# Kernel optimization log

Hardware: AMD Instinct MI355X
Metric: run time of the kernel (lower is better)

Reference implementation:

```python
import jax, jax.numpy as jnp
import numpy as np

T, N, E, F_IN, C = 8, 50000, 800000, 64, 64


def setup_inputs() -> dict:
    key = jax.random.key(0)
    ks = jax.random.split(key, 32)
    inp = {
        "x": jax.random.normal(ks[0], (T, N, F_IN), dtype=jnp.float32),
        "edge_index": jax.random.randint(ks[1], (2, E), 0, N, dtype=jnp.int32),
        "edge_weight": jax.random.uniform(ks[2], (E,), dtype=jnp.float32),
    }
    s = 0.05
    names = ["xz", "hz", "xr", "hr", "xh", "hh"]
    for i, nm in enumerate(names):
        cin = F_IN if nm[0] == "x" else C
        inp[f"W{nm}0"] = jax.random.normal(ks[3 + 3 * i], (cin, C), dtype=jnp.float32) * s
        inp[f"W{nm}1"] = jax.random.normal(ks[4 + 3 * i], (cin, C), dtype=jnp.float32) * s
        inp[f"b{nm}"] = jax.random.normal(ks[5 + 3 * i], (C,), dtype=jnp.float32) * s
    inp["W_lin"] = jax.random.normal(ks[30], (C, 1), dtype=jnp.float32) * s
    inp["b_lin"] = jax.random.normal(ks[31], (1,), dtype=jnp.float32) * s
    return inp


def reference(x, edge_index, edge_weight,
              Wxz0, Wxz1, bxz, Whz0, Whz1, bhz,
              Wxr0, Wxr1, bxr, Whr0, Whr1, bhr,
              Wxh0, Wxh1, bxh, Whh0, Whh1, bhh,
              W_lin, b_lin):
    src, dst = edge_index[0], edge_index[1]
    n = x.shape[1]
    # sym-normalized L_hat = -D^{-1/2} A D^{-1/2} (ChebConv, lambda_max=2)
    deg = jnp.zeros((n,), x.dtype).at[src].add(edge_weight)
    dinv = jnp.where(deg > 0, jax.lax.rsqrt(jnp.maximum(deg, 1e-12)), 0.0)
    nw = -edge_weight * dinv[src] * dinv[dst]  # (E,)

    def cheb(v, W0, W1, b):
        # K=2 Chebyshev: v @ W0 + (L_hat v) @ W1 + b ; v: (T, N, Cin)
        msgs = nw[None, :, None] * v[:, src, :]          # (T, E, Cin)
        tx1 = jnp.zeros_like(v).at[:, dst, :].add(msgs)  # scatter-add over nodes
        return v @ W0 + tx1 @ W1 + b

    H = jnp.zeros(x.shape[:2] + (Whz0.shape[0],), x.dtype)  # H=None -> zeros
    Z = jax.nn.sigmoid(cheb(x, Wxz0, Wxz1, bxz) + cheb(H, Whz0, Whz1, bhz))
    R = jax.nn.sigmoid(cheb(x, Wxr0, Wxr1, bxr) + cheb(H, Whr0, Whr1, bhr))
    Ht = jnp.tanh(cheb(x, Wxh0, Wxh1, bxh) + cheb(R * H, Whh0, Whh1, bhh))
    H = Z * H + (1.0 - Z) * Ht
    h = jax.nn.relu(H)
    return h @ W_lin + b_lin
```

## Files before the change

kernel.cpp:

```cpp
#include <hip/hip_runtime.h>

#define T_ 8
#define N_ 50000
#define E_ 800000
#define C_ 64
#define OVF_CAP 131072
#define NB 196
#define NBLK 256
#define EPB 3125
#define SCN (2 * NB * NBLK)
#define SCAN_TILES 49

typedef __attribute__((ext_vector_type(8))) short bf16x8;
typedef __attribute__((ext_vector_type(4))) float f32x4;

__device__ inline short f2bf(float f) {
    union { float f; unsigned int u; } v; v.f = f;
    unsigned int u = v.u + 0x7FFFu + ((v.u >> 16) & 1u);
    return (short)(u >> 16);
}
__device__ inline float bf2f_lo(unsigned int u) {
    union { unsigned int u; float f; } v; v.u = u << 16;
    return v.f;
}
__device__ inline float bf2f_hi(unsigned int u) {
    union { unsigned int u; float f; } v; v.u = u & 0xffff0000u;
    return v.f;
}

__device__ inline void xcvt_step(int id, const float* __restrict__ x,
                                 unsigned short* __restrict__ xb) {
    int c8 = id & 7;
    int t = (id >> 3) & 7;
    int n = id >> 6;
    const float* xr = x + ((long long)t * N_ + n) * C_ + c8 * 8;
    float4 a = *(const float4*)(xr);
    float4 b = *(const float4*)(xr + 4);
    bf16x8 o;
    o[0] = f2bf(a.x); o[1] = f2bf(a.y); o[2] = f2bf(a.z); o[3] = f2bf(a.w);
    o[4] = f2bf(b.x); o[5] = f2bf(b.y); o[6] = f2bf(b.z); o[7] = f2bf(b.w);
    *(bf16x8*)(xb + (long long)id * 8) = o;
}

__global__ __launch_bounds__(256) void prep_kernel(
        const int* __restrict__ src, const int* __restrict__ dst,
        int* __restrict__ counts,
        const float* __restrict__ x, unsigned short* __restrict__ xb,
        const float* __restrict__ Wz0, const float* __restrict__ Wz1,
        const float* __restrict__ Wh0, const float* __restrict__ Wh1,
        short* __restrict__ swz) {
    if (blockIdx.x < NBLK) {
        __shared__ int h[2 * NB];
        int t = threadIdx.x;
        for (int i = t; i < 2 * NB; i += 256) h[i] = 0;
        __syncthreads();
        int e0 = blockIdx.x * EPB;
        for (int j = t; j < EPB; j += 256) {
            int e = e0 + j;
            atomicAdd(&h[src[e] >> 8], 1);
            atomicAdd(&h[NB + (dst[e] >> 8)], 1);
        }
        __syncthreads();
        for (int i = t; i < 2 * NB; i += 256)
            counts[i * NBLK + blockIdx.x] = h[i];
    } else if (blockIdx.x < NBLK + 12500) {
        int id = (blockIdx.x - NBLK) * 256 + threadIdx.x;
        xcvt_step(id, x, xb);
    } else {
        int idx = (blockIdx.x - NBLK - 12500) * 256 + threadIdx.x;
        int j = idx & 7;
        int lane = (idx >> 3) & 63;
        int kb = (idx >> 9) & 1;
        int c = (idx >> 10) & 3;
        int mat = idx >> 12;
        const float* W = (mat == 0) ? Wz0 : (mat == 1) ? Wz1 : (mat == 2) ? Wh0 : Wh1;
        int k = kb * 32 + (lane >> 4) * 8 + j;
        int n = c * 16 + (lane & 15);
        swz[idx] = f2bf(W[k * 64 + n]);
    }
}

__global__ __launch_bounds__(1024) void scan_a_kernel(int* __restrict__ cnts,
                                                      int* __restrict__ tsum) {
    __shared__ int wsum[16];
    int tid = threadIdx.x, lane = tid & 63, wid = tid >> 6;
    int i0 = blockIdx.x * 2048 + tid * 2;
    int v0 = cnts[i0], v1 = cnts[i0 + 1];
    int orig = v0 + v1;
    int v = orig;
#pragma unroll
    for (int off = 1; off < 64; off <<= 1) {
        int u = __shfl_up(v, off);
        if (lane >= off) v += u;
    }
    if (lane == 63) wsum[wid] = v;
    __syncthreads();
    if (wid == 0) {
        int s = (lane < 16) ? wsum[lane] : 0;
#pragma unroll
        for (int off = 1; off < 16; off <<= 1) {
            int u = __shfl_up(s, off);
            if (lane >= off) s += u;
        }
        if (lane < 16) wsum[lane] = s;
    }
    __syncthreads();
    int wpre = wid ? wsum[wid - 1] : 0;
    int ex = wpre + v - orig;
    cnts[i0] = ex;
    cnts[i0 + 1] = ex + v0;
    if (tid == 0) tsum[blockIdx.x] = wsum[15];
}

__global__ __launch_bounds__(1024) void scan_b_kernel(const int* __restrict__ tsum,
                                                      int* __restrict__ cnts,
                                                      int* __restrict__ ovfcnt) {
    __shared__ int soff[SCAN_TILES];
    int tid = threadIdx.x, lane = tid & 63, wid = tid >> 6;
    if (blockIdx.x == 0 && tid == 0) *ovfcnt = 0;
    if (wid == 0) {
        int own = (lane < SCAN_TILES) ? tsum[lane] : 0;
        int s = own;
#pragma unroll
        for (int off = 1; off < 64; off <<= 1) {
            int u = __shfl_up(s, off);
            if (lane >= off) s += u;
        }
        if (lane < SCAN_TILES) soff[lane] = s - own;
    }
    __syncthreads();
    int off = soff[blockIdx.x];
    int i0 = blockIdx.x * 2048 + tid;
    cnts[i0] += off;
    cnts[i0 + 1024] += off;
}

__global__ __launch_bounds__(1024) void scatter_kernel(
        const int* __restrict__ src, const int* __restrict__ dst,
        const float* __restrict__ w, const int* __restrict__ scn,
        int2* __restrict__ rec) {
    __shared__ int h[512];
    __shared__ int delta[512];
    __shared__ int wsum[8];
    __shared__ int2 lrec[2 * EPB];
    int t = threadIdx.x, lane = t & 63, wid = t >> 6;
    int c = blockIdx.x;
    if (t < 512) h[t] = 0;
    __syncthreads();
    int e0 = c * EPB;
    for (int j = t; j < EPB; j += 1024) {
        int e = e0 + j;
        atomicAdd(&h[src[e] >> 8], 1);
        atomicAdd(&h[NB + (dst[e] >> 8)], 1);
    }
    __syncthreads();
    int v = (t < 512) ? h[t] : 0;
    int s2 = v;
#pragma unroll
    for (int off = 1; off < 64; off <<= 1) {
        int u = __shfl_up(s2, off);
        if (lane >= off) s2 += u;
    }
    if (lane == 63 && wid < 8) wsum[wid] = s2;
    __syncthreads();
    if (t == 0) {
        int r = 0;
#pragma unroll
        for (int i = 0; i < 8; ++i) { int x2 = wsum[i]; wsum[i] = r; r += x2; }
    }
    __syncthreads();
    int ex = (t < 512) ? (wsum[wid] + s2 - v) : 0;
    int gb = (t < 2 * NB) ? scn[t * NBLK + c] : 0;
    __syncthreads();
    if (t < 512) { delta[t] = gb - ex; h[t] = ex; }
    __syncthreads();
    int lb196 = h[NB];
    __syncthreads();
    for (int j = t; j < EPB; j += 1024) {
        int e = e0 + j;
        int s = src[e], d = dst[e];
        int wv = __float_as_int(w[e]);
        int p0 = atomicAdd(&h[s >> 8], 1);
        lrec[p0] = make_int2(s, wv);
        int p1 = atomicAdd(&h[NB + (d >> 8)], 1);
        lrec[p1] = make_int2(s | ((d & 255) << 16) | ((d >> 8) << 24), wv);
    }
    __syncthreads();
    for (int j = t; j < 2 * EPB; j += 1024) {
        int2 r = lrec[j];
        int i = (j >= lb196) ? (NB + ((unsigned)r.x >> 24)) : ((r.x & 0xffff) >> 8);
        rec[delta[i] + j] = r;
    }
}

__global__ __launch_bounds__(1024) void degw_kernel(
        const int2* __restrict__ rec, const int* __restrict__ scn,
        float* __restrict__ degw) {
    __shared__ float acc[256];
    int t = threadIdx.x, b = blockIdx.x;
    if (t < 256) acc[t] = 0.f;
    __syncthreads();
    int s0 = scn[b * NBLK];
    int s1 = scn[(b + 1) * NBLK];
    for (int j = s0 + t; j < s1; j += 1024) {
        int2 r = rec[j];
        atomicAdd(&acc[r.x & 255], __int_as_float(r.y));
    }
    __syncthreads();
    int node = b * 256 + t;
    if (t < 256 && node < N_) degw[node] = acc[t];
}

__global__ __launch_bounds__(1024) void esbuild_kernel(
        const int2* __restrict__ rec, const int* __restrict__ scn,
        const float* __restrict__ degw, int* __restrict__ cnt,
        int2* __restrict__ es, int cap,
        int* __restrict__ ovfcnt, int4* __restrict__ ovf) {
    __shared__ int cl[256];
    __shared__ float di[256];
    int t = threadIdx.x, b = blockIdx.x;
    int node = b * 256 + t;
    if (t < 256) {
        cl[t] = 0;
        float dd = (node < N_) ? degw[node] : 0.f;
        di[t] = dd > 0.f ? rsqrtf(fmaxf(dd, 1e-12f)) : 0.f;
    }
    __syncthreads();
    int s0 = scn[(NB + b) * NBLK];
    int s1 = (b == NB - 1) ? 2 * E_ : scn[(NB + b + 1) * NBLK];
    for (int j = s0 + t; j < s1; j += 1024) {
        int2 r = rec[j];
        int s = r.x & 0xffff;
        int dl = (r.x >> 16) & 255;
        float ds = degw[s];
        float is = ds > 0.f ? rsqrtf(fmaxf(ds, 1e-12f)) : 0.f;
        float nwv = -__int_as_float(r.y) * is * di[dl];
        int rank = atomicAdd(&cl[dl], 1);
        int d = b * 256 + dl;
        if (rank < cap) {
            es[d * cap + rank] = make_int2(s, __float_as_int(nwv));
        } else {
            int op = atomicAdd(ovfcnt, 1);
            if (op < OVF_CAP) ovf[op] = make_int4(d, s, __float_as_int(nwv), 0);
        }
    }
    __syncthreads();
    if (t < 256 && node < N_) cnt[node] = cl[t];
}

#define ACC8(W, V)                                                       \
    acc[0] += (W) * bf2f_lo((V).x); acc[1] += (W) * bf2f_hi((V).x);      \
    acc[2] += (W) * bf2f_lo((V).y); acc[3] += (W) * bf2f_hi((V).y);      \
    acc[4] += (W) * bf2f_lo((V).z); acc[5] += (W) * bf2f_hi((V).z);      \
    acc[6] += (W) * bf2f_lo((V).w); acc[7] += (W) * bf2f_hi((V).w);

__global__ __launch_bounds__(256) void gather_node_kernel(
        const int* __restrict__ cnt, const int2* __restrict__ es, int cap,
        const int* __restrict__ ovfcnt, const int4* __restrict__ ovf,
        const unsigned short* __restrict__ xb, const short* __restrict__ swz,
        const float* __restrict__ bxz, const float* __restrict__ bhz,
        const float* __restrict__ bxh, const float* __restrict__ bhh,
        const float* __restrict__ Wlin, const float* __restrict__ blin,
        float* __restrict__ out, int boff) {
    __shared__ unsigned short ltx[32 * 72];
    __shared__ float laz[2][16][65];

    int lane = threadIdx.x & 63;
    int wid = threadIdx.x >> 6;
    int base = (blockIdx.x + boff) * 4;

    {
        int d = base + wid;
        int t = lane >> 3;
        int oct = lane & 7;
        int2 pk = (lane < cap) ? es[d * cap + lane] : make_int2(0, 0);
        int m = cnt[d];
        int mb = m < cap ? m : cap;

        float acc[8] = {0.f, 0.f, 0.f, 0.f, 0.f, 0.f, 0.f, 0.f};
        const unsigned short* xbase = xb + lane * 8;
        int k = 0;
        for (; k + 3 < mb; k += 4) {
            int s0 = __shfl(pk.x, k);
            int s1 = __shfl(pk.x, k + 1);
            int s2 = __shfl(pk.x, k + 2);
            int s3 = __shfl(pk.x, k + 3);
            uint4 v0 = *(const uint4*)(xbase + (long long)s0 * 512);
            uint4 v1 = *(const uint4*)(xbase + (long long)s1 * 512);
            uint4 v2 = *(const uint4*)(xbase + (long long)s2 * 512);
            uint4 v3 = *(const uint4*)(xbase + (long long)s3 * 512);
            float w0 = __int_as_float(__shfl(pk.y, k));
            float w1 = __int_as_float(__shfl(pk.y, k + 1));
            float w2 = __int_as_float(__shfl(pk.y, k + 2));
            float w3 = __int_as_float(__shfl(pk.y, k + 3));
            ACC8(w0, v0);
            ACC8(w1, v1);
            ACC8(w2, v2);
            ACC8(w3, v3);
        }
        for (; k < mb; ++k) {
            int s0 = __shfl(pk.x, k);
            float w0 = __int_as_float(__shfl(pk.y, k));
            uint4 v0 = *(const uint4*)(xbase + (long long)s0 * 512);
            ACC8(w0, v0);
        }
        if (m > cap) {
            int oc = *ovfcnt;
            if (oc > OVF_CAP) oc = OVF_CAP;
            for (int i = 0; i < oc; ++i) {
                int4 o = ovf[i];
                if (o.x == d) {
                    float w0 = __int_as_float(o.z);
                    uint4 v0 = *(const uint4*)(xbase + (long long)o.y * 512);
                    ACC8(w0, v0);
                }
            }
        }
        uint4 ob;
        ob.x = (unsigned int)(unsigned short)f2bf(acc[0]) |
               ((unsigned int)(unsigned short)f2bf(acc[1]) << 16);
        ob.y = (unsigned int)(unsigned short)f2bf(acc[2]) |
               ((unsigned int)(unsigned short)f2bf(acc[3]) << 16);
        ob.z = (unsigned int)(unsigned short)f2bf(acc[4]) |
               ((unsigned int)(unsigned short)f2bf(acc[5]) << 16);
        ob.w = (unsigned int)(unsigned short)f2bf(acc[6]) |
               ((unsigned int)(unsigned short)f2bf(acc[7]) << 16);
        int r = wid * 8 + t;
        *(uint4*)(ltx + r * 72 + oct * 8) = ob;
    }
    __syncthreads();

    int mt = wid >> 1;
    int g = wid & 1;
    int c16 = lane & 15;
    int kq = lane >> 4;
    int r_blk = mt * 16 + c16;
    const unsigned short* xr = xb + (long long)(base * 8 + r_blk) * C_ + kq * 8;
    bf16x8 ax0 = *(const bf16x8*)(xr);
    bf16x8 ax1 = *(const bf16x8*)(xr + 32);
    bf16x8 at0 = *(const bf16x8*)(ltx + r_blk * 72 + kq * 8);
    bf16x8 at1 = *(const bf16x8*)(ltx + r_blk * 72 + 32 + kq * 8);

    const float* bA = g ? bxh : bxz;
    const float* bB = g ? bhh : bhz;
    const short* wA = swz + (2 * g) * 4096 + lane * 8;
    const short* wB = swz + (2 * g + 1) * 4096 + lane * 8;

    f32x4 a4[4];
#pragma unroll
    for (int c = 0; c < 4; ++c) {
        int col = c * 16 + c16;
        float bv = bA[col] + bB[col];
        a4[c] = (f32x4){bv, bv, bv, bv};
    }
#pragma unroll
    for (int c = 0; c < 4; ++c) {
        bf16x8 bA0 = *(const bf16x8*)(wA + (c * 2 + 0) * 512);
        bf16x8 bA1 = *(const bf16x8*)(wA + (c * 2 + 1) * 512);
        bf16x8 bB0 = *(const bf16x8*)(wB + (c * 2 + 0) * 512);
        bf16x8 bB1 = *(const bf16x8*)(wB + (c * 2 + 1) * 512);
        a4[c] = __builtin_amdgcn_mfma_f32_16x16x32_bf16(ax0, bA0, a4[c], 0, 0, 0);
        a4[c] = __builtin_amdgcn_mfma_f32_16x16x32_bf16(ax1, bA1, a4[c], 0, 0, 0);
        a4[c] = __builtin_amdgcn_mfma_f32_16x16x32_bf16(at0, bB0, a4[c], 0, 0, 0);
        a4[c] = __builtin_amdgcn_mfma_f32_16x16x32_bf16(at1, bB1, a4[c], 0, 0, 0);
    }

    if (g == 0) {
#pragma unroll
        for (int c = 0; c < 4; ++c)
#pragma unroll
            for (int r = 0; r < 4; ++r)
                laz[mt][kq * 4 + r][c * 16 + c16] = a4[c][r];
    }
    __syncthreads();
    if (g == 1) {
        float part[4] = {0.f, 0.f, 0.f, 0.f};
#pragma unroll
        for (int c = 0; c < 4; ++c) {
            int col = c * 16 + c16;
            float wl = Wlin[col];
#pragma unroll
            for (int r = 0; r < 4; ++r) {
                float a = laz[mt][kq * 4 + r][col];
                float b = a4[c][r];
                float z = 1.f / (1.f + __expf(-a));
                float aa = fabsf(b);
                float e = __expf(-2.f * aa);
                float ht = copysignf((1.f - e) / (1.f + e), b);
                float h = fmaxf((1.f - z) * ht, 0.f);
                part[r] += h * wl;
            }
        }
#pragma unroll
        for (int m = 1; m <= 8; m <<= 1) {
#pragma unroll
            for (int r = 0; r < 4; ++r) part[r] += __shfl_xor(part[r], m);
        }
        if (c16 == 0) {
            float bl = blin[0];
#pragma unroll
            for (int r = 0; r < 4; ++r) {
                int rb = mt * 16 + kq * 4 + r;
                out[(long long)(rb & 7) * N_ + base + (rb >> 3)] = part[r] + bl;
            }
        }
    }
}

extern "C" void kernel_launch(void* const* d_in, const int* in_sizes, int n_in,
                              void* d_out, int out_size, void* d_ws, size_t ws_size,
                              hipStream_t stream) {
    const float* x    = (const float*)d_in[0];
    const int*   ei   = (const int*)d_in[1];
    const float* w    = (const float*)d_in[2];
    const float* Wxz0 = (const float*)d_in[3];
    const float* Wxz1 = (const float*)d_in[4];
    const float* bxz  = (const float*)d_in[5];
    const float* bhz  = (const float*)d_in[8];
    const float* Wxh0 = (const float*)d_in[15];
    const float* Wxh1 = (const float*)d_in[16];
    const float* bxh  = (const float*)d_in[17];
    const float* bhh  = (const float*)d_in[20];
    const float* Wlin = (const float*)d_in[21];
    const float* blin = (const float*)d_in[22];
    float* out = (float*)d_out;

    const int* src = ei;
    const int* dst = ei + E_;

    char* ws = (char*)d_ws;
    size_t off = 0;
    auto alloc = [&](size_t bytes) {
        char* p = ws + off;
        off = (off + bytes + 511) & ~(size_t)511;
        return p;
    };
    short* swz         = (short*)alloc(4 * 4096 * sizeof(short));
    float* degw        = (float*)alloc((size_t)N_ * 4);
    int*   cnt         = (int*)alloc((size_t)N_ * 4);
    int*   ovfcnt      = (int*)alloc(512);
    int4*  ovf         = (int4*)alloc((size_t)OVF_CAP * 16);
    int*   counts      = (int*)alloc((size_t)SCN * 4);
    int*   tsum        = (int*)alloc((size_t)SCAN_TILES * 4);
    int2*  rec         = (int2*)alloc((size_t)2 * E_ * 8);
    unsigned short* xb = (unsigned short*)alloc((size_t)T_ * N_ * C_ * 2);
    size_t fixed = off;

    int cap = 16;
    for (int c : {64, 48, 32, 24}) {
        if (fixed + (size_t)N_ * c * 8 + 512 <= ws_size) { cap = c; break; }
    }
    int2* es = (int2*)alloc((size_t)N_ * cap * 8);

    prep_kernel<<<NBLK + 12500 + 64, 256, 0, stream>>>(
        src, dst, counts, x, xb, Wxz0, Wxz1, Wxh0, Wxh1, swz);

    scan_a_kernel<<<SCAN_TILES, 1024, 0, stream>>>(counts, tsum);
    scan_b_kernel<<<SCAN_TILES, 1024, 0, stream>>>(tsum, counts, ovfcnt);

    scatter_kernel<<<NBLK, 1024, 0, stream>>>(src, dst, w, counts, rec);

    degw_kernel<<<NB, 1024, 0, stream>>>(rec, counts, degw);

    esbuild_kernel<<<NB, 1024, 0, stream>>>(rec, counts, degw, cnt,
                                            es, cap, ovfcnt, ovf);

    gather_node_kernel<<<6250, 256, 0, stream>>>(
        cnt, es, cap, ovfcnt, ovf, xb, swz,
        bxz, bhz, bxh, bhh, Wlin, blin, out, 0);
    gather_node_kernel<<<6250, 256, 0, stream>>>(
        cnt, es, cap, ovfcnt, ovf, xb, swz,
        bxz, bhz, bxh, bhh, Wlin, blin, out, 6250);
}
```

Baseline: 367.9 us.

## Replace global scan with atomic bucket cursors and fuse scatter into prep

```diff
diff --git a/kernel.cpp b/kernel.cpp
--- a/kernel.cpp
+++ b/kernel.cpp
@@ -4,12 +4,11 @@
 #define N_ 50000
 #define E_ 800000
 #define C_ 64
-#define OVF_CAP 131072
+#define OVF_CAP 65536
 #define NB 196
 #define NBLK 256
 #define EPB 3125
-#define SCN (2 * NB * NBLK)
-#define SCAN_TILES 49
+#define BCAP 6144
 
 typedef __attribute__((ext_vector_type(8))) short bf16x8;
 typedef __attribute__((ext_vector_type(4))) float f32x4;
@@ -42,32 +41,89 @@
     *(bf16x8*)(xb + (long long)id * 8) = o;
 }
 
-__global__ __launch_bounds__(256) void prep_kernel(
+__global__ __launch_bounds__(1024) void mega_prep_kernel(
         const int* __restrict__ src, const int* __restrict__ dst,
-        int* __restrict__ counts,
+        const float* __restrict__ w,
+        unsigned long long* __restrict__ cursor,
+        int* __restrict__ ovfAcnt, int4* __restrict__ ovfA,
+        int2* __restrict__ rec,
         const float* __restrict__ x, unsigned short* __restrict__ xb,
         const float* __restrict__ Wz0, const float* __restrict__ Wz1,
         const float* __restrict__ Wh0, const float* __restrict__ Wh1,
         short* __restrict__ swz) {
+    int t = threadIdx.x;
     if (blockIdx.x < NBLK) {
-        __shared__ int h[2 * NB];
-        int t = threadIdx.x;
-        for (int i = t; i < 2 * NB; i += 256) h[i] = 0;
-        __syncthreads();
-        int e0 = blockIdx.x * EPB;
-        for (int j = t; j < EPB; j += 256) {
+        __shared__ int h[512];
+        __shared__ int delta[512];
+        __shared__ int wsum[16];
+        __shared__ unsigned long long gres[NB];
+        __shared__ int2 lrec[2 * EPB];
+        int lane = t & 63, wid = t >> 6;
+        int c = blockIdx.x;
+        if (t < 512) h[t] = 0;
+        __syncthreads();
+        int e0 = c * EPB;
+        for (int j = t; j < EPB; j += 1024) {
             int e = e0 + j;
             atomicAdd(&h[src[e] >> 8], 1);
             atomicAdd(&h[NB + (dst[e] >> 8)], 1);
         }
         __syncthreads();
-        for (int i = t; i < 2 * NB; i += 256)
-            counts[i * NBLK + blockIdx.x] = h[i];
-    } else if (blockIdx.x < NBLK + 12500) {
-        int id = (blockIdx.x - NBLK) * 256 + threadIdx.x;
+        int v = (t < 512) ? h[t] : 0;
+        if (t < NB) {
+            unsigned long long add =
+                ((unsigned long long)(unsigned)h[NB + t] << 32) | (unsigned)h[t];
+            gres[t] = atomicAdd(&cursor[t], add);
+        }
+        int s2 = v;
+#pragma unroll
+        for (int off = 1; off < 64; off <<= 1) {
+            int u = __shfl_up(s2, off);
+            if (lane >= off) s2 += u;
+        }
+        if (lane == 63) wsum[wid] = s2;
+        __syncthreads();
+        if (t == 0) {
+            int r = 0;
+#pragma unroll
+            for (int i = 0; i < 16; ++i) { int x2 = wsum[i]; wsum[i] = r; r += x2; }
+        }
+        __syncthreads();
+        int ex = wsum[wid] + s2 - v;
+        if (t < 512) {
+            int gb = (t < NB) ? (int)(gres[t] & 0xffffffffULL)
+                              : (int)(gres[t - NB] >> 32);
+            delta[t] = gb - ex;
+            h[t] = ex;
+        }
+        __syncthreads();
+        for (int j = t; j < EPB; j += 1024) {
+            int e = e0 + j;
+            int s = src[e], d = dst[e];
+            int wv = __float_as_int(w[e]);
+            int p0 = atomicAdd(&h[s >> 8], 1);
+            lrec[p0] = make_int2(s, wv);
+            int p1 = atomicAdd(&h[NB + (d >> 8)], 1);
+            lrec[p1] = make_int2(s | ((d & 255) << 16) | ((d >> 8) << 24), wv);
+        }
+        __syncthreads();
+        for (int j = t; j < 2 * EPB; j += 1024) {
+            int2 r = lrec[j];
+            int isd = (j >= EPB);
+            int i = isd ? (NB + (int)((unsigned)r.x >> 24)) : ((r.x & 0xffff) >> 8);
+            int rel = delta[i] + j;
+            if (rel < BCAP) {
+                rec[(long long)i * BCAP + rel] = r;
+            } else {
+                int op = atomicAdd(ovfAcnt, 1);
+                if (op < OVF_CAP) ovfA[op] = make_int4(isd, r.x, r.y, 0);
+            }
+        }
+    } else if (blockIdx.x < NBLK + 3125) {
+        int id = (blockIdx.x - NBLK) * 1024 + t;
         xcvt_step(id, x, xb);
     } else {
-        int idx = (blockIdx.x - NBLK - 12500) * 256 + threadIdx.x;
+        int idx = (blockIdx.x - NBLK - 3125) * 1024 + t;
         int j = idx & 7;
         int lane = (idx >> 3) & 63;
         int kb = (idx >> 9) & 1;
@@ -80,131 +136,32 @@
     }
 }
 
-__global__ __launch_bounds__(1024) void scan_a_kernel(int* __restrict__ cnts,
-                                                      int* __restrict__ tsum) {
-    __shared__ int wsum[16];
-    int tid = threadIdx.x, lane = tid & 63, wid = tid >> 6;
-    int i0 = blockIdx.x * 2048 + tid * 2;
-    int v0 = cnts[i0], v1 = cnts[i0 + 1];
-    int orig = v0 + v1;
-    int v = orig;
-#pragma unroll
-    for (int off = 1; off < 64; off <<= 1) {
-        int u = __shfl_up(v, off);
-        if (lane >= off) v += u;
-    }
-    if (lane == 63) wsum[wid] = v;
-    __syncthreads();
-    if (wid == 0) {
-        int s = (lane < 16) ? wsum[lane] : 0;
-#pragma unroll
-        for (int off = 1; off < 16; off <<= 1) {
-            int u = __shfl_up(s, off);
-            if (lane >= off) s += u;
-        }
-        if (lane < 16) wsum[lane] = s;
-    }
-    __syncthreads();
-    int wpre = wid ? wsum[wid - 1] : 0;
-    int ex = wpre + v - orig;
-    cnts[i0] = ex;
-    cnts[i0 + 1] = ex + v0;
-    if (tid == 0) tsum[blockIdx.x] = wsum[15];
-}
-
-__global__ __launch_bounds__(1024) void scan_b_kernel(const int* __restrict__ tsum,
-                                                      int* __restrict__ cnts,
-                                                      int* __restrict__ ovfcnt) {
-    __shared__ int soff[SCAN_TILES];
-    int tid = threadIdx.x, lane = tid & 63, wid = tid >> 6;
-    if (blockIdx.x == 0 && tid == 0) *ovfcnt = 0;
-    if (wid == 0) {
-        int own = (lane < SCAN_TILES) ? tsum[lane] : 0;
-        int s = own;
-#pragma unroll
-        for (int off = 1; off < 64; off <<= 1) {
-            int u = __shfl_up(s, off);
-            if (lane >= off) s += u;
-        }
-        if (lane < SCAN_TILES) soff[lane] = s - own;
-    }
-    __syncthreads();
-    int off = soff[blockIdx.x];
-    int i0 = blockIdx.x * 2048 + tid;
-    cnts[i0] += off;
-    cnts[i0 + 1024] += off;
-}
-
-__global__ __launch_bounds__(1024) void scatter_kernel(
-        const int* __restrict__ src, const int* __restrict__ dst,
-        const float* __restrict__ w, const int* __restrict__ scn,
-        int2* __restrict__ rec) {
-    __shared__ int h[512];
-    __shared__ int delta[512];
-    __shared__ int wsum[8];
-    __shared__ int2 lrec[2 * EPB];
-    int t = threadIdx.x, lane = t & 63, wid = t >> 6;
-    int c = blockIdx.x;
-    if (t < 512) h[t] = 0;
-    __syncthreads();
-    int e0 = c * EPB;
-    for (int j = t; j < EPB; j += 1024) {
-        int e = e0 + j;
-        atomicAdd(&h[src[e] >> 8], 1);
-        atomicAdd(&h[NB + (dst[e] >> 8)], 1);
-    }
-    __syncthreads();
-    int v = (t < 512) ? h[t] : 0;
-    int s2 = v;
-#pragma unroll
-    for (int off = 1; off < 64; off <<= 1) {
-        int u = __shfl_up(s2, off);
-        if (lane >= off) s2 += u;
-    }
-    if (lane == 63 && wid < 8) wsum[wid] = s2;
-    __syncthreads();
-    if (t == 0) {
-        int r = 0;
-#pragma unroll
-        for (int i = 0; i < 8; ++i) { int x2 = wsum[i]; wsum[i] = r; r += x2; }
-    }
-    __syncthreads();
-    int ex = (t < 512) ? (wsum[wid] + s2 - v) : 0;
-    int gb = (t < 2 * NB) ? scn[t * NBLK + c] : 0;
-    __syncthreads();
-    if (t < 512) { delta[t] = gb - ex; h[t] = ex; }
-    __syncthreads();
-    int lb196 = h[NB];
-    __syncthreads();
-    for (int j = t; j < EPB; j += 1024) {
-        int e = e0 + j;
-        int s = src[e], d = dst[e];
-        int wv = __float_as_int(w[e]);
-        int p0 = atomicAdd(&h[s >> 8], 1);
-        lrec[p0] = make_int2(s, wv);
-        int p1 = atomicAdd(&h[NB + (d >> 8)], 1);
-        lrec[p1] = make_int2(s | ((d & 255) << 16) | ((d >> 8) << 24), wv);
-    }
-    __syncthreads();
-    for (int j = t; j < 2 * EPB; j += 1024) {
-        int2 r = lrec[j];
-        int i = (j >= lb196) ? (NB + ((unsigned)r.x >> 24)) : ((r.x & 0xffff) >> 8);
-        rec[delta[i] + j] = r;
-    }
-}
-
 __global__ __launch_bounds__(1024) void degw_kernel(
-        const int2* __restrict__ rec, const int* __restrict__ scn,
+        const int2* __restrict__ rec, const unsigned long long* __restrict__ cursor,
+        const int* __restrict__ ovfAcnt, const int4* __restrict__ ovfA,
         float* __restrict__ degw) {
     __shared__ float acc[256];
     int t = threadIdx.x, b = blockIdx.x;
     if (t < 256) acc[t] = 0.f;
     __syncthreads();
-    int s0 = scn[b * NBLK];
-    int s1 = scn[(b + 1) * NBLK];
-    for (int j = s0 + t; j < s1; j += 1024) {
-        int2 r = rec[j];
+    int fill = (int)(cursor[b] & 0xffffffffULL);
+    if (fill > BCAP) fill = BCAP;
+    const int2* base = rec + (long long)b * BCAP;
+    for (int j = t; j < fill; j += 1024) {
+        int2 r = base[j];
         atomicAdd(&acc[r.x & 255], __int_as_float(r.y));
+    }
+    __syncthreads();
+    if (t == 0) {
+        int oc = *ovfAcnt;
+        if (oc > OVF_CAP) oc = OVF_CAP;
+        for (int i = 0; i < oc; ++i) {
+            int4 o = ovfA[i];
+            if (o.x == 0) {
+                int s = o.y & 0xffff;
+                if ((s >> 8) == b) acc[s & 255] += __int_as_float(o.z);
+            }
+        }
     }
     __syncthreads();
     int node = b * 256 + t;
@@ -212,10 +169,11 @@
 }
 
 __global__ __launch_bounds__(1024) void esbuild_kernel(
-        const int2* __restrict__ rec, const int* __restrict__ scn,
+        const int2* __restrict__ rec, const unsigned long long* __restrict__ cursor,
         const float* __restrict__ degw, int* __restrict__ cnt,
         int2* __restrict__ es, int cap,
-        int* __restrict__ ovfcnt, int4* __restrict__ ovf) {
+        const int* __restrict__ ovfAcnt, const int4* __restrict__ ovfA,
+        int* __restrict__ ovfBcnt, int4* __restrict__ ovfB) {
     __shared__ int cl[256];
     __shared__ float di[256];
     int t = threadIdx.x, b = blockIdx.x;
@@ -226,10 +184,11 @@
         di[t] = dd > 0.f ? rsqrtf(fmaxf(dd, 1e-12f)) : 0.f;
     }
     __syncthreads();
-    int s0 = scn[(NB + b) * NBLK];
-    int s1 = (b == NB - 1) ? 2 * E_ : scn[(NB + b + 1) * NBLK];
-    for (int j = s0 + t; j < s1; j += 1024) {
-        int2 r = rec[j];
+    int fill = (int)(cursor[b] >> 32);
+    if (fill > BCAP) fill = BCAP;
+    const int2* base = rec + (long long)(NB + b) * BCAP;
+    for (int j = t; j < fill; j += 1024) {
+        int2 r = base[j];
         int s = r.x & 0xffff;
         int dl = (r.x >> 16) & 255;
         float ds = degw[s];
@@ -240,8 +199,34 @@
         if (rank < cap) {
             es[d * cap + rank] = make_int2(s, __float_as_int(nwv));
         } else {
-            int op = atomicAdd(ovfcnt, 1);
-            if (op < OVF_CAP) ovf[op] = make_int4(d, s, __float_as_int(nwv), 0);
+            int op = atomicAdd(ovfBcnt, 1);
+            if (op < OVF_CAP) ovfB[op] = make_int4(d, s, __float_as_int(nwv), 0);
+        }
+    }
+    __syncthreads();
+    if (t == 0) {
+        int oc = *ovfAcnt;
+        if (oc > OVF_CAP) oc = OVF_CAP;
+        for (int i = 0; i < oc; ++i) {
+            int4 o = ovfA[i];
+            if (o.x == 1) {
+                int dh = (int)((unsigned)o.y >> 24);
+                if (dh == b) {
+                    int s = o.y & 0xffff;
+                    int dl = (o.y >> 16) & 255;
+                    float ds = degw[s];
+                    float is = ds > 0.f ? rsqrtf(fmaxf(ds, 1e-12f)) : 0.f;
+                    float nwv = -__int_as_float(o.z) * is * di[dl];
+                    int rank = cl[dl]++;
+                    int d = b * 256 + dl;
+                    if (rank < cap) {
+                        es[d * cap + rank] = make_int2(s, __float_as_int(nwv));
+                    } else {
+                        int op = atomicAdd(ovfBcnt, 1);
+                        if (op < OVF_CAP) ovfB[op] = make_int4(d, s, __float_as_int(nwv), 0);
+                    }
+                }
+            }
         }
     }
     __syncthreads();
@@ -261,13 +246,13 @@
         const float* __restrict__ bxz, const float* __restrict__ bhz,
         const float* __restrict__ bxh, const float* __restrict__ bhh,
         const float* __restrict__ Wlin, const float* __restrict__ blin,
-        float* __restrict__ out, int boff) {
+        float* __restrict__ out) {
     __shared__ unsigned short ltx[32 * 72];
     __shared__ float laz[2][16][65];
 
     int lane = threadIdx.x & 63;
     int wid = threadIdx.x >> 6;
-    int base = (blockIdx.x + boff) * 4;
+    int base = blockIdx.x * 4;
 
     {
         int d = base + wid;
@@ -438,11 +423,13 @@
     short* swz         = (short*)alloc(4 * 4096 * sizeof(short));
     float* degw        = (float*)alloc((size_t)N_ * 4);
     int*   cnt         = (int*)alloc((size_t)N_ * 4);
-    int*   ovfcnt      = (int*)alloc(512);
-    int4*  ovf         = (int4*)alloc((size_t)OVF_CAP * 16);
-    int*   counts      = (int*)alloc((size_t)SCN * 4);
-    int*   tsum        = (int*)alloc((size_t)SCAN_TILES * 4);
-    int2*  rec         = (int2*)alloc((size_t)2 * E_ * 8);
+    char*  ctr         = (char*)alloc(4096);
+    unsigned long long* cursor = (unsigned long long*)ctr;
+    int*   ovfAcnt     = (int*)(ctr + 2048);
+    int*   ovfBcnt     = (int*)(ctr + 2560);
+    int4*  ovfA        = (int4*)alloc((size_t)OVF_CAP * 16);
+    int4*  ovfB        = (int4*)alloc((size_t)OVF_CAP * 16);
+    int2*  rec         = (int2*)alloc((size_t)2 * NB * BCAP * 8);
     unsigned short* xb = (unsigned short*)alloc((size_t)T_ * N_ * C_ * 2);
     size_t fixed = off;
 
@@ -452,23 +439,18 @@
     }
     int2* es = (int2*)alloc((size_t)N_ * cap * 8);
 
-    prep_kernel<<<NBLK + 12500 + 64, 256, 0, stream>>>(
-        src, dst, counts, x, xb, Wxz0, Wxz1, Wxh0, Wxh1, swz);
-
-    scan_a_kernel<<<SCAN_TILES, 1024, 0, stream>>>(counts, tsum);
-    scan_b_kernel<<<SCAN_TILES, 1024, 0, stream>>>(tsum, counts, ovfcnt);
-
-    scatter_kernel<<<NBLK, 1024, 0, stream>>>(src, dst, w, counts, rec);
-
-    degw_kernel<<<NB, 1024, 0, stream>>>(rec, counts, degw);
-
-    esbuild_kernel<<<NB, 1024, 0, stream>>>(rec, counts, degw, cnt,
-                                            es, cap, ovfcnt, ovf);
-
-    gather_node_kernel<<<6250, 256, 0, stream>>>(
-        cnt, es, cap, ovfcnt, ovf, xb, swz,
-        bxz, bhz, bxh, bhh, Wlin, blin, out, 0);
-    gather_node_kernel<<<6250, 256, 0, stream>>>(
-        cnt, es, cap, ovfcnt, ovf, xb, swz,
-        bxz, bhz, bxh, bhh, Wlin, blin, out, 6250);
-}
+    hipMemsetAsync(ctr, 0, 4096, stream);
+
+    mega_prep_kernel<<<NBLK + 3125 + 16, 1024, 0, stream>>>(
+        src, dst, w, cursor, ovfAcnt, ovfA, rec,
+        x, xb, Wxz0, Wxz1, Wxh0, Wxh1, swz);
+
+    degw_kernel<<<NB, 1024, 0, stream>>>(rec, cursor, ovfAcnt, ovfA, degw);
+
+    esbuild_kernel<<<NB, 1024, 0, stream>>>(rec, cursor, degw, cnt, es, cap,
+                                            ovfAcnt, ovfA, ovfBcnt, ovfB);
+
+    gather_node_kernel<<<N_ / 4, 256, 0, stream>>>(
+        cnt, es, cap, ovfBcnt, ovfB, xb, swz,
+        bxz, bhz, bxh, bhh, Wlin, blin, out);
+}
```

After: 347.1 us. 5.7% less time.
